# Kernel tuning notes

Measured on AMD Instinct MI355X. Metric: run time of the kernel, lower is better.

The kernel has to match this reference:

```python
import jax, jax.numpy as jnp
import numpy as np

T, H, I, E, K = 8192, 2048, 768, 16, 2  # tokens, hidden, moe_intermediate, experts, top_k


def setup_inputs() -> dict:
    key = jax.random.key(0)
    k0, k1, k2, k3, k4 = jax.random.split(key, 5)
    return {
        "hidden_states": jax.random.normal(k0, (T, H), jnp.float32),
        "top_k_index": jax.random.randint(k1, (T, K), 0, E),
        "top_k_weights": jax.random.uniform(k2, (T, K), jnp.float32),
        "gate_up_proj": jax.random.normal(k3, (E, 2 * I, H), jnp.float32) * 0.02,
        "down_proj": jax.random.normal(k4, (E, H, I), jnp.float32) * 0.02,
    }


def reference(hidden_states, top_k_index, top_k_weights, gate_up_proj, down_proj):
    num_experts = gate_up_proj.shape[0]
    # combine[t, e] = sum over k of top_k_weights[t, k] where top_k_index[t, k] == e
    # (duplicated expert picks sum their weights, matching torch index_add_ semantics)
    onehot = jax.nn.one_hot(top_k_index, num_experts, dtype=hidden_states.dtype)  # [T, K, E]
    combine = jnp.einsum("tke,tk->te", onehot, top_k_weights)                      # [T, E]
    out = jnp.zeros_like(hidden_states)
    # fixed small loop over structurally distinct experts; unselected tokens get weight 0
    for e in range(num_experts):
        gate_up = hidden_states @ gate_up_proj[e].T        # [T, 2I]
        gate, up = jnp.split(gate_up, 2, axis=-1)
        act = jax.nn.silu(gate) * up                       # SwiGLU, [T, I]
        down = act @ down_proj[e].T                        # [T, H]
        out = out + down * combine[:, e:e + 1]
    return out
```

## Files before the change

### kernel.cpp

```cpp
#include <hip/hip_runtime.h>

#define TT 8192
#define HH 2048
#define II 768
#define NE 16
#define TOPK 2
#define CAP 16384

typedef float f32x4 __attribute__((ext_vector_type(4)));
typedef float f32x8 __attribute__((ext_vector_type(8)));
typedef short bf16x8 __attribute__((ext_vector_type(8)));
typedef unsigned short ushort8 __attribute__((ext_vector_type(8)));
typedef unsigned short ushort16 __attribute__((ext_vector_type(16)));

__device__ __forceinline__ unsigned short f2bf(float f) {
    unsigned u = __builtin_bit_cast(unsigned, f);
    u += 0x7fffu + ((u >> 16) & 1u);
    return (unsigned short)(u >> 16);
}

__device__ __forceinline__ float bf2f(unsigned short u) {
    return __builtin_bit_cast(float, (unsigned)u << 16);
}

__device__ __forceinline__ void glds16(const void* g, void* l) {
    __builtin_amdgcn_global_load_lds((const __attribute__((address_space(1))) void*)g,
                                     (__attribute__((address_space(3))) void*)l, 16, 0, 0);
}

__global__ void cast_route_kernel(const float* __restrict__ gup, const float* __restrict__ hs,
                                  const int* __restrict__ tki, const float* __restrict__ tkw,
                                  unsigned short* __restrict__ wg1,
                                  unsigned short* __restrict__ hsb,
                                  int* __restrict__ counts, int* __restrict__ poffs,
                                  int* __restrict__ ntot, int* __restrict__ tmap,
                                  int* __restrict__ toks, float* __restrict__ wts) {
    const int bid = blockIdx.x;
    if (bid == 0) {
        __shared__ int lcnt[NE];
        const int tid = threadIdx.x;
        if (tid < NE) lcnt[tid] = 0;
        __syncthreads();
        for (int t = tid; t < TT; t += 256) {
            #pragma unroll
            for (int k = 0; k < TOPK; ++k) {
                int e = tki[t * TOPK + k];
                int p = atomicAdd(&lcnt[e], 1);
                toks[e * CAP + p] = t | (k << 15);
                wts[e * CAP + p] = tkw[t * TOPK + k];
            }
        }
        __syncthreads();
        if (tid == 0) {
            int s = 0, nt = 0;
            for (int e = 0; e < NE; ++e) {
                counts[e] = lcnt[e];
                poffs[e] = s;
                int ct = (lcnt[e] + 127) >> 7;
                for (int m = 0; m < ct; ++m) tmap[nt++] = e | (m << 8);
                s += ct << 7;
            }
            poffs[NE] = s;
            ntot[0] = nt;
        }
    } else if (bid < 12289) {
        size_t gid0 = (size_t)(bid - 1) * 512 + threadIdx.x * 2;
        int sc = gid0 & 7;
        int r = (gid0 >> 3) & 255;
        int kt = (gid0 >> 11) & 31;
        int rest = (int)(gid0 >> 16);
        int it = rest % 6;
        int e = rest / 6;
        int grow = (r < 128) ? (it * 128 + r) : (II + it * 128 + (r - 128));
        const float* rp = &gup[((size_t)e * (2 * II) + grow) * HH + kt * 64];
        int c0 = sc ^ (r & 7), c1 = c0 ^ 1;
        const float4 a0 = *reinterpret_cast<const float4*>(rp + c0 * 8);
        const float4 a1 = *reinterpret_cast<const float4*>(rp + c0 * 8 + 4);
        const float4 b0 = *reinterpret_cast<const float4*>(rp + c1 * 8);
        const float4 b1 = *reinterpret_cast<const float4*>(rp + c1 * 8 + 4);
        ushort16 o;
        o[0] = f2bf(a0.x); o[1] = f2bf(a0.y); o[2]  = f2bf(a0.z); o[3]  = f2bf(a0.w);
        o[4] = f2bf(a1.x); o[5] = f2bf(a1.y); o[6]  = f2bf(a1.z); o[7]  = f2bf(a1.w);
        o[8] = f2bf(b0.x); o[9] = f2bf(b0.y); o[10] = f2bf(b0.z); o[11] = f2bf(b0.w);
        o[12] = f2bf(b1.x); o[13] = f2bf(b1.y); o[14] = f2bf(b1.z); o[15] = f2bf(b1.w);
        *reinterpret_cast<ushort16*>(&wg1[gid0 * 8]) = o;
    } else {
        size_t i0 = ((size_t)(bid - 12289) * 256 + threadIdx.x) * 4;
        const float4* src = reinterpret_cast<const float4*>(hs);
        const float4 v0 = src[i0], v1 = src[i0 + 1], v2 = src[i0 + 2], v3 = src[i0 + 3];
        ushort16 o;
        o[0] = f2bf(v0.x); o[1] = f2bf(v0.y); o[2]  = f2bf(v0.z); o[3]  = f2bf(v0.w);
        o[4] = f2bf(v1.x); o[5] = f2bf(v1.y); o[6]  = f2bf(v1.z); o[7]  = f2bf(v1.w);
        o[8] = f2bf(v2.x); o[9] = f2bf(v2.y); o[10] = f2bf(v2.z); o[11] = f2bf(v2.w);
        o[12] = f2bf(v3.x); o[13] = f2bf(v3.y); o[14] = f2bf(v3.z); o[15] = f2bf(v3.w);
        *reinterpret_cast<ushort16*>(&hsb[i0 * 4]) = o;
    }
}

__global__ __launch_bounds__(256, 2) void gemm1_kernel(
    const unsigned short* __restrict__ hsb, const unsigned short* __restrict__ wg1,
    const float* __restrict__ dwn, unsigned short* __restrict__ wg2,
    const int* __restrict__ counts, const int* __restrict__ poffs,
    const int* __restrict__ ntotp, const int* __restrict__ tmap,
    const int* __restrict__ toks, unsigned short* __restrict__ actT) {
    const int b = blockIdx.x;
    if (b >= 864) {
        size_t gid0 = (size_t)(b - 864) * 512 + threadIdx.x * 2;
        int sc = gid0 & 7;
        int r = (gid0 >> 3) & 127;
        int kt = (int)((gid0 >> 10) % 12);
        int rest = (int)(gid0 / (12 << 10));
        int ht = rest & 15;
        int e = rest >> 4;
        int hrow = ht * 128 + r;
        const float* rp = &dwn[((size_t)e * HH + hrow) * II + kt * 64];
        int c0 = sc ^ (r & 7), c1 = c0 ^ 1;
        const float4 a0 = *reinterpret_cast<const float4*>(rp + c0 * 8);
        const float4 a1 = *reinterpret_cast<const float4*>(rp + c0 * 8 + 4);
        const float4 b0 = *reinterpret_cast<const float4*>(rp + c1 * 8);
        const float4 b1 = *reinterpret_cast<const float4*>(rp + c1 * 8 + 4);
        ushort16 o;
        o[0] = f2bf(a0.x); o[1] = f2bf(a0.y); o[2]  = f2bf(a0.z); o[3]  = f2bf(a0.w);
        o[4] = f2bf(a1.x); o[5] = f2bf(a1.y); o[6]  = f2bf(a1.z); o[7]  = f2bf(a1.w);
        o[8] = f2bf(b0.x); o[9] = f2bf(b0.y); o[10] = f2bf(b0.z); o[11] = f2bf(b0.w);
        o[12] = f2bf(b1.x); o[13] = f2bf(b1.y); o[14] = f2bf(b1.z); o[15] = f2bf(b1.w);
        *reinterpret_cast<ushort16*>(&wg2[gid0 * 8]) = o;
        return;
    }
    const int w = (b & 7) * 108 + (b >> 3);
    const int ibt = w / 144;
    const int gt = w % 144;
    if (gt >= ntotp[0]) return;
    const int ent = tmap[gt];
    const int e = ent & 255;
    const int mbase = (ent >> 8) << 7;
    const int cnt = counts[e];
    const int tid = threadIdx.x;
    const int lane = tid & 63;
    const int wid = tid >> 6;
    const int wm = wid >> 1, wn = wid & 1;

    __shared__ unsigned short sA[128 * 64];
    __shared__ unsigned short sB[256 * 64];
    __shared__ int s_tok[128];

    if (tid < 128) {
        int r = mbase + tid;
        s_tok[tid] = toks[e * CAP + ((r < cnt) ? r : (cnt - 1))] & 0x1FFF;
    }
    __syncthreads();

    size_t abase[4];
    #pragma unroll
    for (int it = 0; it < 4; ++it) {
        int idx = it * 256 + tid;
        int r = idx >> 3, sc = idx & 7;
        abase[it] = (size_t)s_tok[r] * HH + ((sc ^ (r & 7)) << 3);
    }
    const unsigned short* bbase = wg1 + ((size_t)(e * 6 + ibt) << 19) + (size_t)tid * 8;

    f32x4 accg[4][4], accu[4][4];
    #pragma unroll
    for (int m = 0; m < 4; ++m)
        #pragma unroll
        for (int n = 0; n < 4; ++n) {
            accg[m][n] = (f32x4){0.f, 0.f, 0.f, 0.f};
            accu[m][n] = (f32x4){0.f, 0.f, 0.f, 0.f};
        }

    const int lrow = lane & 15;
    const int lk8 = (lane >> 4) << 3;

    for (int k0 = 0; k0 < HH; k0 += 64) {
        #pragma unroll
        for (int it = 0; it < 4; ++it)
            glds16(hsb + abase[it] + k0, (char*)sA + it * 4096 + wid * 1024);
        const unsigned short* bk = bbase + ((size_t)(k0 >> 6) * 16384);
        #pragma unroll
        for (int it = 0; it < 8; ++it)
            glds16(bk + it * 2048, (char*)sB + it * 4096 + wid * 1024);
        __syncthreads();
        #pragma unroll
        for (int ks = 0; ks < 2; ++ks) {
            bf16x8 af[4], bg[4], bu[4];
            #pragma unroll
            for (int m = 0; m < 4; ++m) {
                int row = wm * 64 + m * 16 + lrow;
                af[m] = *reinterpret_cast<const bf16x8*>(
                    &sA[(row << 6) + ((ks * 32 + lk8) ^ ((row & 7) << 3))]);
            }
            #pragma unroll
            for (int n = 0; n < 4; ++n) {
                int rg = wn * 64 + n * 16 + lrow;
                bg[n] = *reinterpret_cast<const bf16x8*>(
                    &sB[(rg << 6) + ((ks * 32 + lk8) ^ ((rg & 7) << 3))]);
                int ru = rg + 128;
                bu[n] = *reinterpret_cast<const bf16x8*>(
                    &sB[(ru << 6) + ((ks * 32 + lk8) ^ ((ru & 7) << 3))]);
            }
            #pragma unroll
            for (int m = 0; m < 4; ++m)
                #pragma unroll
                for (int n = 0; n < 4; ++n) {
                    accg[m][n] = __builtin_amdgcn_mfma_f32_16x16x32_bf16(af[m], bg[n], accg[m][n], 0, 0, 0);
                    accu[m][n] = __builtin_amdgcn_mfma_f32_16x16x32_bf16(af[m], bu[n], accu[m][n], 0, 0, 0);
                }
        }
        __syncthreads();
    }

    const int mt = (poffs[e] + mbase) >> 7;
    #pragma unroll
    for (int m = 0; m < 4; ++m)
        #pragma unroll
        for (int n = 0; n < 4; ++n)
            #pragma unroll
            for (int j = 0; j < 4; ++j) {
                int row = wm * 64 + m * 16 + ((lane >> 4) << 2) + j;
                if (mbase + row < cnt) {
                    int c = wn * 64 + n * 16 + lrow;
                    int ktile = ibt * 2 + (c >> 6);
                    int cc = c & 63;
                    float g = accg[m][n][j], u = accu[m][n][j];
                    float a = (g / (1.f + __expf(-g))) * u;
                    actT[((size_t)(mt * 12 + ktile) * 128 + row) * 64 +
                         (((cc >> 3) ^ (row & 7)) << 3) + (cc & 7)] = f2bf(a);
                }
            }
}

__global__ __launch_bounds__(256) void gemm2_kernel(
    const unsigned short* __restrict__ actT, const unsigned short* __restrict__ wg2,
    const int* __restrict__ counts, const int* __restrict__ poffs,
    const int* __restrict__ ntotp, const int* __restrict__ tmap,
    const int* __restrict__ toks, const float* __restrict__ wts,
    unsigned short* __restrict__ partial) {
    const int b = blockIdx.x;
    const int w = (b & 7) * 288 + (b >> 3);
    const int ht = w / 144;
    const int gt = w % 144;
    if (gt >= ntotp[0]) return;
    const int ent = tmap[gt];
    const int e = ent & 255;
    const int mbase = (ent >> 8) << 7;
    const int cnt = counts[e];
    const int tid = threadIdx.x;
    const int lane = tid & 63;
    const int wid = tid >> 6;
    const int wm = wid >> 1, wn = wid & 1;

    __shared__ unsigned short sA[128 * 64];
    __shared__ unsigned short sB[128 * 64];
    __shared__ int s_tok[128];
    __shared__ float s_wt[128];

    if (tid < 128) {
        int r = mbase + tid;
        int rc = (r < cnt) ? r : (cnt - 1);
        s_tok[tid] = toks[e * CAP + rc];
        s_wt[tid] = wts[e * CAP + rc];
    }

    const int mt = (poffs[e] + mbase) >> 7;
    const unsigned short* abase = actT + (size_t)(mt * 12) * 8192 + (size_t)tid * 8;
    const unsigned short* bbase = wg2 + (size_t)((e * 16 + ht) * 12) * 8192 + (size_t)tid * 8;

    f32x4 acc[4][4];
    #pragma unroll
    for (int m = 0; m < 4; ++m)
        #pragma unroll
        for (int n = 0; n < 4; ++n) acc[m][n] = (f32x4){0.f, 0.f, 0.f, 0.f};

    const int lrow = lane & 15;
    const int lk8 = (lane >> 4) << 3;

    for (int kt = 0; kt < 12; ++kt) {
        #pragma unroll
        for (int it = 0; it < 4; ++it)
            glds16(abase + (size_t)kt * 8192 + it * 2048, (char*)sA + it * 4096 + wid * 1024);
        #pragma unroll
        for (int it = 0; it < 4; ++it)
            glds16(bbase + (size_t)kt * 8192 + it * 2048, (char*)sB + it * 4096 + wid * 1024);
        __syncthreads();
        #pragma unroll
        for (int ks = 0; ks < 2; ++ks) {
            bf16x8 af[4], bb[4];
            #pragma unroll
            for (int m = 0; m < 4; ++m) {
                int row = wm * 64 + m * 16 + lrow;
                af[m] = *reinterpret_cast<const bf16x8*>(
                    &sA[(row << 6) + ((ks * 32 + lk8) ^ ((row & 7) << 3))]);
            }
            #pragma unroll
            for (int n = 0; n < 4; ++n) {
                int rb = wn * 64 + n * 16 + lrow;
                bb[n] = *reinterpret_cast<const bf16x8*>(
                    &sB[(rb << 6) + ((ks * 32 + lk8) ^ ((rb & 7) << 3))]);
            }
            #pragma unroll
            for (int m = 0; m < 4; ++m)
                #pragma unroll
                for (int n = 0; n < 4; ++n)
                    acc[m][n] = __builtin_amdgcn_mfma_f32_16x16x32_bf16(af[m], bb[n], acc[m][n], 0, 0, 0);
        }
        __syncthreads();
    }

    #pragma unroll
    for (int m = 0; m < 4; ++m) {
        int row = wm * 64 + m * 16 + ((lane >> 4) << 2);
        #pragma unroll
        for (int j = 0; j < 4; ++j) {
            if (mbase + row + j < cnt) {
                int v = s_tok[row + j];
                size_t rbase = ((size_t)(v >> 15) * TT + (v & 0x1FFF)) * HH + ht * 128;
                float w = s_wt[row + j];
                #pragma unroll
                for (int n = 0; n < 4; ++n)
                    partial[rbase + wn * 64 + n * 16 + lrow] = f2bf(acc[m][n][j] * w);
            }
        }
    }
}

__global__ void combine_kernel(const unsigned short* __restrict__ partial, float* __restrict__ out) {
    size_t i = ((size_t)blockIdx.x * blockDim.x + threadIdx.x) * 2;
    const ushort8* pa = reinterpret_cast<const ushort8*>(partial);
    const ushort8* pb = reinterpret_cast<const ushort8*>(partial + (size_t)TT * HH);
    const ushort8 a0 = pa[i], a1 = pa[i + 1];
    const ushort8 b0 = pb[i], b1 = pb[i + 1];
    f32x8 o0, o1;
    #pragma unroll
    for (int j = 0; j < 8; ++j) { o0[j] = bf2f(a0[j]) + bf2f(b0[j]); o1[j] = bf2f(a1[j]) + bf2f(b1[j]); }
    *reinterpret_cast<f32x8*>(&out[i * 8]) = o0;
    *reinterpret_cast<f32x8*>(&out[i * 8 + 8]) = o1;
}

extern "C" void kernel_launch(void* const* d_in, const int* in_sizes, int n_in,
                              void* d_out, int out_size, void* d_ws, size_t ws_size,
                              hipStream_t stream) {
    const float* hs = (const float*)d_in[0];
    const int* tki = (const int*)d_in[1];
    const float* tkw = (const float*)d_in[2];
    const float* gup = (const float*)d_in[3];
    const float* dwn = (const float*)d_in[4];
    float* out = (float*)d_out;

    char* ws = (char*)d_ws;
    int* counts = (int*)(ws);
    int* poffs = (int*)(ws + 128);
    int* ntot = (int*)(ws + 224);
    int* tmap = (int*)(ws + 256);
    int* toks = (int*)(ws + 1024);
    float* wts = (float*)(ws + 1024 + (size_t)CAP * NE * 4);
    unsigned short* hsb = (unsigned short*)(ws + 2098176);
    unsigned short* wg1 = (unsigned short*)(ws + 35652608);
    unsigned short* wg2 = (unsigned short*)(ws + 136315904);
    unsigned short* actT = (unsigned short*)(ws + 186647552);
    unsigned short* partial = (unsigned short*)(ws + 2098176);

    cast_route_kernel<<<16385, 256, 0, stream>>>(gup, hs, tki, tkw, wg1, hsb,
                                                 counts, poffs, ntot, tmap, toks, wts);
    gemm1_kernel<<<7008, 256, 0, stream>>>(hsb, wg1, dwn, wg2,
                                           counts, poffs, ntot, tmap, toks, actT);
    gemm2_kernel<<<2304, 256, 0, stream>>>(actT, wg2, counts, poffs, ntot, tmap, toks, wts, partial);
    combine_kernel<<<(TT * HH / 16) / 256, 256, 0, stream>>>(partial, out);
}
```

Baseline: 343.7 us.

## Double-buffer gemm1 LDS tiles with 512-thread blocks and overlapped prefetch

Reworks the first grouped GEMM to use 512-thread blocks with eight waves arranged 2x4, each computing a narrower 64x32 gate/up sub-tile. The A and B tiles are now double-buffered in LDS, so the next K-tile's global-to-LDS loads are issued while the current tile's MFMAs run, with explicit waitcnt and barriers in place of full syncthreads. MFMA sections also raise wave priority via s_setprio. This targets exposed global-load latency in the K loop, at the cost of doubled LDS use (about 96KB per block), lower occupancy, and less register reuse per wave. The weight-cast tail blocks and the launch grid are resized to match.

```diff
diff --git a/kernel.cpp b/kernel.cpp
--- a/kernel.cpp
+++ b/kernel.cpp
@@ -97,7 +97,7 @@
     }
 }
 
-__global__ __launch_bounds__(256, 2) void gemm1_kernel(
+__global__ __launch_bounds__(512) void gemm1_kernel(
     const unsigned short* __restrict__ hsb, const unsigned short* __restrict__ wg1,
     const float* __restrict__ dwn, unsigned short* __restrict__ wg2,
     const int* __restrict__ counts, const int* __restrict__ poffs,
@@ -105,7 +105,7 @@
     const int* __restrict__ toks, unsigned short* __restrict__ actT) {
     const int b = blockIdx.x;
     if (b >= 864) {
-        size_t gid0 = (size_t)(b - 864) * 512 + threadIdx.x * 2;
+        size_t gid0 = (size_t)(b - 864) * 1024 + threadIdx.x * 2;
         int sc = gid0 & 7;
         int r = (gid0 >> 3) & 127;
         int kt = (int)((gid0 >> 10) % 12);
@@ -138,10 +138,11 @@
     const int tid = threadIdx.x;
     const int lane = tid & 63;
     const int wid = tid >> 6;
-    const int wm = wid >> 1, wn = wid & 1;
-
-    __shared__ unsigned short sA[128 * 64];
-    __shared__ unsigned short sB[256 * 64];
+    const int wm = wid >> 2;
+    const int wn = wid & 3;
+
+    __shared__ unsigned short sA0[128 * 64], sA1[128 * 64];
+    __shared__ unsigned short sB0[256 * 64], sB1[256 * 64];
     __shared__ int s_tok[128];
 
     if (tid < 128) {
@@ -150,20 +151,20 @@
     }
     __syncthreads();
 
-    size_t abase[4];
-    #pragma unroll
-    for (int it = 0; it < 4; ++it) {
-        int idx = it * 256 + tid;
+    size_t abase[2];
+    #pragma unroll
+    for (int it = 0; it < 2; ++it) {
+        int idx = it * 512 + tid;
         int r = idx >> 3, sc = idx & 7;
         abase[it] = (size_t)s_tok[r] * HH + ((sc ^ (r & 7)) << 3);
     }
     const unsigned short* bbase = wg1 + ((size_t)(e * 6 + ibt) << 19) + (size_t)tid * 8;
 
-    f32x4 accg[4][4], accu[4][4];
+    f32x4 accg[4][2], accu[4][2];
     #pragma unroll
     for (int m = 0; m < 4; ++m)
         #pragma unroll
-        for (int n = 0; n < 4; ++n) {
+        for (int n = 0; n < 2; ++n) {
             accg[m][n] = (f32x4){0.f, 0.f, 0.f, 0.f};
             accu[m][n] = (f32x4){0.f, 0.f, 0.f, 0.f};
         }
@@ -171,54 +172,86 @@
     const int lrow = lane & 15;
     const int lk8 = (lane >> 4) << 3;
 
-    for (int k0 = 0; k0 < HH; k0 += 64) {
-        #pragma unroll
-        for (int it = 0; it < 4; ++it)
-            glds16(hsb + abase[it] + k0, (char*)sA + it * 4096 + wid * 1024);
-        const unsigned short* bk = bbase + ((size_t)(k0 >> 6) * 16384);
-        #pragma unroll
-        for (int it = 0; it < 8; ++it)
-            glds16(bk + it * 2048, (char*)sB + it * 4096 + wid * 1024);
-        __syncthreads();
-        #pragma unroll
-        for (int ks = 0; ks < 2; ++ks) {
-            bf16x8 af[4], bg[4], bu[4];
-            #pragma unroll
-            for (int m = 0; m < 4; ++m) {
-                int row = wm * 64 + m * 16 + lrow;
-                af[m] = *reinterpret_cast<const bf16x8*>(
-                    &sA[(row << 6) + ((ks * 32 + lk8) ^ ((row & 7) << 3))]);
-            }
-            #pragma unroll
-            for (int n = 0; n < 4; ++n) {
-                int rg = wn * 64 + n * 16 + lrow;
-                bg[n] = *reinterpret_cast<const bf16x8*>(
-                    &sB[(rg << 6) + ((ks * 32 + lk8) ^ ((rg & 7) << 3))]);
-                int ru = rg + 128;
-                bu[n] = *reinterpret_cast<const bf16x8*>(
-                    &sB[(ru << 6) + ((ks * 32 + lk8) ^ ((ru & 7) << 3))]);
-            }
-            #pragma unroll
-            for (int m = 0; m < 4; ++m)
-                #pragma unroll
-                for (int n = 0; n < 4; ++n) {
-                    accg[m][n] = __builtin_amdgcn_mfma_f32_16x16x32_bf16(af[m], bg[n], accg[m][n], 0, 0, 0);
-                    accu[m][n] = __builtin_amdgcn_mfma_f32_16x16x32_bf16(af[m], bu[n], accu[m][n], 0, 0, 0);
-                }
-        }
-        __syncthreads();
+#define G1_STAGE(SA, SB, kt) do {                                              \
+    _Pragma("unroll")                                                          \
+    for (int it = 0; it < 2; ++it)                                             \
+        glds16(hsb + abase[it] + (size_t)(kt) * 64,                            \
+               (char*)(SA) + it * 8192 + tid * 16);                            \
+    const unsigned short* bk_ = bbase + (size_t)(kt) * 16384;                  \
+    _Pragma("unroll")                                                          \
+    for (int it = 0; it < 4; ++it)                                             \
+        glds16(bk_ + it * 4096, (char*)(SB) + it * 8192 + tid * 16);           \
+} while (0)
+
+#define G1_READ(SA, SB, ks, af, bg, bu) do {                                   \
+    _Pragma("unroll")                                                          \
+    for (int m = 0; m < 4; ++m) {                                              \
+        int row = wm * 64 + m * 16 + lrow;                                     \
+        af[m] = *reinterpret_cast<const bf16x8*>(                              \
+            &(SA)[(row << 6) + (((ks) * 32 + lk8) ^ ((row & 7) << 3))]);       \
+    }                                                                          \
+    _Pragma("unroll")                                                          \
+    for (int n = 0; n < 2; ++n) {                                              \
+        int rg = wn * 32 + n * 16 + lrow;                                      \
+        bg[n] = *reinterpret_cast<const bf16x8*>(                              \
+            &(SB)[(rg << 6) + (((ks) * 32 + lk8) ^ ((rg & 7) << 3))]);         \
+        int ru = rg + 128;                                                     \
+        bu[n] = *reinterpret_cast<const bf16x8*>(                              \
+            &(SB)[(ru << 6) + (((ks) * 32 + lk8) ^ ((ru & 7) << 3))]);         \
+    }                                                                          \
+} while (0)
+
+#define G1_MMA(af, bg, bu) do {                                                \
+    __builtin_amdgcn_s_setprio(1);                                             \
+    _Pragma("unroll")                                                          \
+    for (int m = 0; m < 4; ++m)                                                \
+        _Pragma("unroll")                                                      \
+        for (int n = 0; n < 2; ++n) {                                          \
+            accg[m][n] = __builtin_amdgcn_mfma_f32_16x16x32_bf16(af[m], bg[n], accg[m][n], 0, 0, 0); \
+            accu[m][n] = __builtin_amdgcn_mfma_f32_16x16x32_bf16(af[m], bu[n], accu[m][n], 0, 0, 0); \
+        }                                                                      \
+    __builtin_amdgcn_s_setprio(0);                                             \
+} while (0)
+
+#define G1_TILE(SA, SB, do_stage, kt2) do {                                    \
+    bf16x8 af0[4], bg0[2], bu0[2];                                             \
+    G1_READ(SA, SB, 0, af0, bg0, bu0);                                         \
+    G1_MMA(af0, bg0, bu0);                                                     \
+    bf16x8 af1[4], bg1[2], bu1[2];                                             \
+    G1_READ(SA, SB, 1, af1, bg1, bu1);                                         \
+    asm volatile("s_waitcnt lgkmcnt(0)" ::: "memory");                         \
+    __builtin_amdgcn_s_barrier();                                              \
+    if (do_stage) {                                                            \
+        G1_STAGE(SA, SB, kt2);                                                 \
+        G1_MMA(af1, bg1, bu1);                                                 \
+        asm volatile("s_waitcnt vmcnt(6)" ::: "memory");                       \
+    } else {                                                                   \
+        G1_MMA(af1, bg1, bu1);                                                 \
+        asm volatile("s_waitcnt vmcnt(0)" ::: "memory");                       \
+    }                                                                          \
+    __builtin_amdgcn_s_barrier();                                              \
+} while (0)
+
+    G1_STAGE(sA0, sB0, 0);
+    G1_STAGE(sA1, sB1, 1);
+    asm volatile("s_waitcnt vmcnt(6)" ::: "memory");
+    __builtin_amdgcn_s_barrier();
+    #pragma unroll 1
+    for (int kt = 0; kt < 32; kt += 2) {
+        G1_TILE(sA0, sB0, kt < 30, kt + 2);
+        G1_TILE(sA1, sB1, kt < 29, kt + 3);
     }
 
     const int mt = (poffs[e] + mbase) >> 7;
     #pragma unroll
     for (int m = 0; m < 4; ++m)
         #pragma unroll
-        for (int n = 0; n < 4; ++n)
+        for (int n = 0; n < 2; ++n)
             #pragma unroll
             for (int j = 0; j < 4; ++j) {
                 int row = wm * 64 + m * 16 + ((lane >> 4) << 2) + j;
                 if (mbase + row < cnt) {
-                    int c = wn * 64 + n * 16 + lrow;
+                    int c = wn * 32 + n * 16 + lrow;
                     int ktile = ibt * 2 + (c >> 6);
                     int cc = c & 63;
                     float g = accg[m][n][j], u = accu[m][n][j];
@@ -361,7 +394,7 @@
 
     cast_route_kernel<<<16385, 256, 0, stream>>>(gup, hs, tki, tkw, wg1, hsb,
                                                  counts, poffs, ntot, tmap, toks, wts);
-    gemm1_kernel<<<7008, 256, 0, stream>>>(hsb, wg1, dwn, wg2,
+    gemm1_kernel<<<3936, 512, 0, stream>>>(hsb, wg1, dwn, wg2,
                                            counts, poffs, ntot, tmap, toks, actT);
     gemm2_kernel<<<2304, 256, 0, stream>>>(actT, wg2, counts, poffs, ntot, tmap, toks, wts, partial);
     combine_kernel<<<(TT * HH / 16) / 256, 256, 0, stream>>>(partial, out);
```

Result: slower. 361.7 us (+5.2%).
